# Kernel tuning notes

Measured on AMD Instinct MI355X. Metric: run time of the kernel, lower is better.

## Reference

```python
import jax, jax.numpy as jnp
import numpy as np

D_MODEL = 1024
NUM_HEADS = 16
DEPTH = D_MODEL // NUM_HEADS
NEG_INF = -1e9


def setup_inputs() -> dict:
    key = jax.random.key(0)
    ks = jax.random.split(key, 12)
    B, S = 4, 2048
    scale = 1.0 / np.sqrt(D_MODEL)
    inp = {
        "q": jax.random.normal(ks[0], (B, S, D_MODEL), jnp.float32),
        "k": jax.random.normal(ks[1], (B, S, D_MODEL), jnp.float32),
        "v": jax.random.normal(ks[2], (B, S, D_MODEL), jnp.float32),
        "mask": jax.random.randint(ks[3], (B, 1, 1, S), 0, 2, jnp.int32),
        "wq": jax.random.normal(ks[4], (D_MODEL, D_MODEL), jnp.float32) * scale,
        "bq": jnp.zeros((D_MODEL,), jnp.float32),
        "wk": jax.random.normal(ks[5], (D_MODEL, D_MODEL), jnp.float32) * scale,
        "bk": jnp.zeros((D_MODEL,), jnp.float32),
        "wv": jax.random.normal(ks[6], (D_MODEL, D_MODEL), jnp.float32) * scale,
        "bv": jnp.zeros((D_MODEL,), jnp.float32),
        "wo": jax.random.normal(ks[7], (D_MODEL, D_MODEL), jnp.float32) * scale,
        "bo": jnp.zeros((D_MODEL,), jnp.float32),
    }
    return inp


def _split_heads(x):
    # [B, S, D] -> [B, H, S, depth]
    B, S, _ = x.shape
    return x.reshape(B, S, NUM_HEADS, DEPTH).transpose(0, 2, 1, 3)


def reference(q, k, v, mask, wq, bq, wk, bk, wv, bv, wo, bo):
    B, S, _ = q.shape
    qh = _split_heads(q @ wq + bq)  # [B,H,S,d]
    kh = _split_heads(k @ wk + bk)
    vh = _split_heads(v @ wv + bv)
    logits = jnp.einsum("bhqd,bhkd->bhqk", qh, kh) / jnp.sqrt(
        jnp.asarray(DEPTH, jnp.float32))
    logits = logits + mask.astype(jnp.float32) * NEG_INF
    weights = jax.nn.softmax(logits, axis=-1)
    attn = jnp.einsum("bhqk,bhkd->bhqd", weights, vh)
    attn = attn.transpose(0, 2, 1, 3).reshape(B, S, D_MODEL)
    return attn @ wo + bo
```

## Files before the change

kernel.cpp:

```cpp
#include <hip/hip_runtime.h>

#define SB 4
#define SS 2048
#define SD 1024
#define SH 16

typedef float f32x4 __attribute__((ext_vector_type(4)));
typedef __bf16 bf16x8 __attribute__((ext_vector_type(8)));
typedef short short4v __attribute__((ext_vector_type(4)));
typedef unsigned int uint2v __attribute__((ext_vector_type(2)));

__device__ __forceinline__ unsigned short f2bf_(float x) {
    unsigned u = __builtin_bit_cast(unsigned, x);
    unsigned r = u + 0x7FFFu + ((u >> 16) & 1u);
    return (unsigned short)(r >> 16);
}

#define GL2LDS(g, l) __builtin_amdgcn_global_load_lds( \
    (const __attribute__((address_space(1))) unsigned int*)(g), \
    (__attribute__((address_space(3))) unsigned int*)(l), 16, 0, 0)

__global__ __launch_bounds__(256) void maskprep(
        const int* __restrict__ mk, float* __restrict__ MA, int n) {
    int i = blockIdx.x * 256 + threadIdx.x;
    if (i < n)
        MA[i] = (float)mk[i] * (-1e9f * 1.4426950408889634f) - 8.0f;
}

__global__ __launch_bounds__(256) void transpose4(
        const float* __restrict__ w0, const float* __restrict__ w1,
        const float* __restrict__ w2, const float* __restrict__ w3,
        unsigned short* __restrict__ out) {
    __shared__ unsigned short tile[32][33];
    int zz = blockIdx.z;
    const float* src = (zz == 0) ? w0 : (zz == 1) ? w1 : (zz == 2) ? w2 : w3;
    unsigned short* dst = out + (size_t)zz * 1024 * 1024;
    int x = blockIdx.x * 32 + threadIdx.x;
    int y0 = blockIdx.y * 32;
    for (int j = threadIdx.y; j < 32; j += 8)
        tile[j][threadIdx.x] = f2bf_(src[(size_t)(y0 + j) * 1024 + x]);
    __syncthreads();
    int ox = y0 + threadIdx.x;
    int oy0 = blockIdx.x * 32;
    for (int j = threadIdx.y; j < 32; j += 8)
        dst[(size_t)(oy0 + j) * 1024 + ox] = tile[threadIdx.x][j];
}

__global__ __launch_bounds__(256) void gemm_qkv(
        const float* __restrict__ Aq, const float* __restrict__ Ak,
        const float* __restrict__ Avv, const unsigned short* __restrict__ WT,
        const float* __restrict__ bq, const float* __restrict__ bk,
        const float* __restrict__ bv, unsigned short* __restrict__ Qh,
        unsigned short* __restrict__ Kh, unsigned short* __restrict__ VTr,
        float qscl) {
    __shared__ alignas(16) float Asmf[2][128][32];
    __shared__ alignas(16) unsigned short Bsm[2][128][32];
    const int zone = blockIdx.x >> 6;
    const int m0 = (blockIdx.x & 63) * 128, n0 = blockIdx.y * 128;
    const float* Af = (zone == 0) ? Aq : (zone == 1) ? Ak : Avv;
    const unsigned short* BT = WT + (size_t)zone * 1048576;
    const float* bias = (zone == 0) ? bq : (zone == 1) ? bk : bv;
    const int K = 1024, N = 1024;

    const int lane = threadIdx.x & 63, wid = threadIdx.x >> 6;
    const int wr = wid >> 1, wc = wid & 1;
    const int lr = lane >> 2;
    const int lco = (lane & 3) * 8;
    const int cl = lane & 15, kg = lane >> 4;

    f32x4 acc[4][4] = {};

    auto STAGE = [&](int buf, int k0) {
#pragma unroll
        for (int i = 0; i < 4; ++i) {
            int base = i * 32 + wid * 8;
            int row = base + (lane >> 3);
            int cs = (lane & 7) ^ (row & 7);
            GL2LDS(Af + (size_t)(m0 + row) * K + k0 + cs * 4, &Asmf[buf][base][0]);
        }
#pragma unroll
        for (int i = 0; i < 2; ++i) {
            int base = (i * 4 + wid) * 16;
            GL2LDS(BT + (size_t)(n0 + base + lr) * K + k0 + lco, &Bsm[buf][base][0]);
        }
    };

    STAGE(0, 0);
    __syncthreads();

    for (int k0 = 0; k0 < K; k0 += 32) {
        int cur = (k0 >> 5) & 1;
        if (k0 + 32 < K) STAGE(cur ^ 1, k0 + 32);

        bf16x8 af[4], bfv[4];
#pragma unroll
        for (int mi = 0; mi < 4; ++mi) {
            int r = wr * 64 + mi * 16 + cl;
            const float* Ar = &Asmf[cur][r][0];
            f32x4 a0 = *(const f32x4*)(Ar + ((2 * kg) ^ (r & 7)) * 4);
            f32x4 a1 = *(const f32x4*)(Ar + ((2 * kg + 1) ^ (r & 7)) * 4);
#pragma unroll
            for (int e = 0; e < 4; ++e) {
                af[mi][e] = (__bf16)a0[e];
                af[mi][4 + e] = (__bf16)a1[e];
            }
        }
#pragma unroll
        for (int ni = 0; ni < 4; ++ni)
            bfv[ni] = *(const bf16x8*)&Bsm[cur][wc * 64 + ni * 16 + cl][kg * 8];
#pragma unroll
        for (int mi = 0; mi < 4; ++mi)
#pragma unroll
            for (int ni = 0; ni < 4; ++ni)
                acc[mi][ni] = __builtin_amdgcn_mfma_f32_16x16x32_bf16(
                    af[mi], bfv[ni], acc[mi][ni], 0, 0, 0);
        __syncthreads();
    }

    const int rl = (lane >> 4) * 4;
    float os = (zone == 0) ? qscl : 1.0f;
#pragma unroll
    for (int mi = 0; mi < 4; ++mi) {
#pragma unroll
        for (int ni = 0; ni < 4; ++ni) {
            int row = m0 + wr * 64 + mi * 16 + rl;
            int col = n0 + wc * 64 + ni * 16 + cl;
            float bvv = bias[col];
            f32x4 v = acc[mi][ni];
            if (zone < 2) {
                unsigned short* C = (zone == 0) ? Qh : Kh;
#pragma unroll
                for (int j = 0; j < 4; ++j)
                    C[(size_t)(row + j) * N + col] = f2bf_((v[j] + bvv) * os);
            } else {
                int bb = row >> 11, s = row & 2047;
                short4v pk;
#pragma unroll
                for (int j = 0; j < 4; ++j)
                    pk[j] = (short)f2bf_(v[j] + bvv);
                *(short4v*)&VTr[((size_t)(bb * 1024 + col)) * 2048 + s] = pk;
            }
        }
    }
}

__global__ __launch_bounds__(256) void gemm_out(
        const unsigned short* __restrict__ Ab, const unsigned short* __restrict__ BT,
        const float* __restrict__ bias, float* __restrict__ C,
        int M, int N, int K) {
    __shared__ alignas(16) unsigned short Asmb[2][128][32];
    __shared__ alignas(16) unsigned short Bsm[2][128][32];
    const int m0 = blockIdx.x * 128, n0 = blockIdx.y * 128;
    const int lane = threadIdx.x & 63, wid = threadIdx.x >> 6;
    const int wr = wid >> 1, wc = wid & 1;
    const int lr = lane >> 2;
    const int lco = (lane & 3) * 8;
    const int cl = lane & 15, kg = lane >> 4;

    f32x4 acc[4][4] = {};

    auto STAGE = [&](int buf, int k0) {
#pragma unroll
        for (int i = 0; i < 2; ++i) {
            int base = (i * 4 + wid) * 16;
            GL2LDS(Ab + (size_t)(m0 + base + lr) * K + k0 + lco, &Asmb[buf][base][0]);
            GL2LDS(BT + (size_t)(n0 + base + lr) * K + k0 + lco, &Bsm[buf][base][0]);
        }
    };

    STAGE(0, 0);
    __syncthreads();

    for (int k0 = 0; k0 < K; k0 += 32) {
        int cur = (k0 >> 5) & 1;
        if (k0 + 32 < K) STAGE(cur ^ 1, k0 + 32);

        bf16x8 af[4], bfv[4];
#pragma unroll
        for (int mi = 0; mi < 4; ++mi)
            af[mi] = *(const bf16x8*)&Asmb[cur][wr * 64 + mi * 16 + cl][kg * 8];
#pragma unroll
        for (int ni = 0; ni < 4; ++ni)
            bfv[ni] = *(const bf16x8*)&Bsm[cur][wc * 64 + ni * 16 + cl][kg * 8];
#pragma unroll
        for (int mi = 0; mi < 4; ++mi)
#pragma unroll
            for (int ni = 0; ni < 4; ++ni)
                acc[mi][ni] = __builtin_amdgcn_mfma_f32_16x16x32_bf16(
                    af[mi], bfv[ni], acc[mi][ni], 0, 0, 0);
        __syncthreads();
    }

    const int rl = (lane >> 4) * 4;
#pragma unroll
    for (int mi = 0; mi < 4; ++mi) {
#pragma unroll
        for (int ni = 0; ni < 4; ++ni) {
            int row = m0 + wr * 64 + mi * 16 + rl;
            int col = n0 + wc * 64 + ni * 16 + cl;
            float bv = bias[col];
            f32x4 v = acc[mi][ni];
#pragma unroll
            for (int j = 0; j < 4; ++j)
                C[(size_t)(row + j) * N + col] = v[j] + bv;
        }
    }
}

__global__ __launch_bounds__(512) void attn_kernel(
        const unsigned short* __restrict__ Qp, const unsigned short* __restrict__ Kp,
        const unsigned short* __restrict__ VT, const float* __restrict__ MA,
        unsigned short* __restrict__ O) {
    __shared__ alignas(16) unsigned short Klds[2][128][64];
    __shared__ alignas(16) unsigned short Vlds[2][64][128];
    const int lane = threadIdx.x & 63, wid = threadIdx.x >> 6;
    const int bh = blockIdx.x;
    const int b = bh >> 4, h = bh & 15;
    const int qt = blockIdx.y;
    const int qrow0 = qt * 256 + wid * 32;
    const int cl = lane & 15, kg = lane >> 4;

    bf16x8 qf[2][2];
#pragma unroll
    for (int qh = 0; qh < 2; ++qh)
#pragma unroll
        for (int kh = 0; kh < 2; ++kh)
            qf[qh][kh] = *(const bf16x8*)&Qp[(size_t)(b * SS + qrow0 + qh * 16 + cl) * SD
                                            + h * 64 + kh * 32 + kg * 8];

    const float* MAb = MA + b * SS;

    f32x4 oacc[2][4] = {};
    f32x4 lsum[2] = {};

    auto STAGE = [&](int buf, int tt) {
        int kt = (tt & 15) * 128;
        {
            int r8 = lane >> 3, c8 = lane & 7;
#pragma unroll
            for (int i = 0; i < 2; ++i) {
                int r = i * 64 + wid * 8 + r8;
                int cs = c8 ^ (r & 7);
                GL2LDS(Kp + (size_t)(b * SS + kt + r) * SD + h * 64 + cs * 8,
                       &Klds[buf][i * 64 + wid * 8][0]);
            }
        }
        {
            int r16 = lane >> 4, c16 = lane & 15;
#pragma unroll
            for (int i = 0; i < 2; ++i) {
                int r = i * 32 + wid * 4 + r16;
                int cs = (c16 & 8) | ((c16 & 7) ^ (r & 7));
                GL2LDS(VT + (size_t)(b * 1024 + h * 64 + r) * 2048 + kt + cs * 8,
                       &Vlds[buf][i * 32 + wid * 4][0]);
            }
        }
    };

    auto QKCOL = [&](int buf, int kt, int cf, f32x4* sv) {
        int r = cf * 16 + cl;
        bf16x8 kf0 = *(const bf16x8*)&Klds[buf][r][((0 + kg) ^ (r & 7)) * 8];
        bf16x8 kf1 = *(const bf16x8*)&Klds[buf][r][((4 + kg) ^ (r & 7)) * 8];
        f32x4 M = *(const f32x4*)&MAb[kt + cf * 16 + 4 * kg];
        __builtin_amdgcn_s_setprio(1);
#pragma unroll
        for (int qh = 0; qh < 2; ++qh) {
            f32x4 s = {};
            s = __builtin_amdgcn_mfma_f32_16x16x32_bf16(kf0, qf[qh][0], s, 0, 0, 0);
            s = __builtin_amdgcn_mfma_f32_16x16x32_bf16(kf1, qf[qh][1], s, 0, 0, 0);
#pragma unroll
            for (int j = 0; j < 4; ++j)
                s[j] = __builtin_amdgcn_exp2f(s[j] + M[j]);
            sv[qh] = s;
            lsum[qh] += s;
        }
        __builtin_amdgcn_s_setprio(0);
    };

    auto STEP = [&](int buf, int t) {
        int kt = t * 128;
#pragma unroll
        for (int ks = 0; ks < 4; ++ks) {
            f32x4 sA[2], sB[2];
            QKCOL(buf, kt, ks, sA);
            QKCOL(buf, kt, ks + 4, sB);
            bf16x8 pa[2];
#pragma unroll
            for (int qh = 0; qh < 2; ++qh) {
                pa[qh][0] = (__bf16)sA[qh][0];
                pa[qh][1] = (__bf16)sA[qh][1];
                pa[qh][2] = (__bf16)sA[qh][2];
                pa[qh][3] = (__bf16)sA[qh][3];
                pa[qh][4] = (__bf16)sB[qh][0];
                pa[qh][5] = (__bf16)sB[qh][1];
                pa[qh][6] = (__bf16)sB[qh][2];
                pa[qh][7] = (__bf16)sB[qh][3];
            }
            __builtin_amdgcn_s_setprio(1);
#pragma unroll
            for (int nf = 0; nf < 4; ++nf) {
                int d = nf * 16 + cl;
                int c16a = 2 * ks + (kg >> 1);
                int c16b = 2 * (ks + 4) + (kg >> 1);
                int cha = (c16a & 8) | ((c16a & 7) ^ (d & 7));
                int chb = (c16b & 8) | ((c16b & 7) ^ (d & 7));
                const char* vb = (const char*)&Vlds[buf][d][0];
                uint2v lo = *(const uint2v*)(vb + cha * 16 + (kg & 1) * 8);
                uint2v hi = *(const uint2v*)(vb + chb * 16 + (kg & 1) * 8);
                bf16x8 vf;
                *(uint2v*)&vf = lo;
                *((uint2v*)&vf + 1) = hi;
#pragma unroll
                for (int qh = 0; qh < 2; ++qh)
                    oacc[qh][nf] = __builtin_amdgcn_mfma_f32_16x16x32_bf16(
                        pa[qh], vf, oacc[qh][nf], 0, 0, 0);
            }
            __builtin_amdgcn_s_setprio(0);
        }
    };

    STAGE(0, 0);
    __syncthreads();
    for (int t = 0; t < 16; ++t) {
        int cur = t & 1;
        STAGE(cur ^ 1, t + 1);
        STEP(cur, t);
        __syncthreads();
    }

    float lfull[2];
#pragma unroll
    for (int qh = 0; qh < 2; ++qh) {
        float l = (lsum[qh][0] + lsum[qh][1]) + (lsum[qh][2] + lsum[qh][3]);
        l += __shfl_xor(l, 16);
        l += __shfl_xor(l, 32);
        lfull[qh] = l;
    }
#pragma unroll
    for (int qh = 0; qh < 2; ++qh) {
#pragma unroll
        for (int j = 0; j < 4; ++j) {
            float inv = 1.0f / __shfl(lfull[qh], 4 * kg + j);
#pragma unroll
            for (int nf = 0; nf < 4; ++nf)
                O[(size_t)(b * SS + qrow0 + qh * 16 + 4 * kg + j) * SD + h * 64 + nf * 16 + cl] =
                    f2bf_(oacc[qh][nf][j] * inv);
        }
    }
}

extern "C" void kernel_launch(void* const* d_in, const int* in_sizes, int n_in,
                              void* d_out, int out_size, void* d_ws, size_t ws_size,
                              hipStream_t stream) {
    const float* q  = (const float*)d_in[0];
    const float* k  = (const float*)d_in[1];
    const float* v  = (const float*)d_in[2];
    const int*   mk = (const int*)d_in[3];
    const float* wq = (const float*)d_in[4];
    const float* bq = (const float*)d_in[5];
    const float* wk = (const float*)d_in[6];
    const float* bk = (const float*)d_in[7];
    const float* wv = (const float*)d_in[8];
    const float* bv = (const float*)d_in[9];
    const float* wo = (const float*)d_in[10];
    const float* bo = (const float*)d_in[11];
    float* out = (float*)d_out;

    char* ws = (char*)d_ws;
    unsigned short* WT  = (unsigned short*)ws;
    unsigned short* X   = (unsigned short*)(ws + 8388608);
    unsigned short* Qh  = (unsigned short*)(ws + 25165824);
    unsigned short* Kh  = (unsigned short*)(ws + 41943040);
    unsigned short* VTr = (unsigned short*)(ws + 58720256);
    float*          MAf = (float*)(ws + 75497472);

    const float QSCL = 0.125f * 1.4426950408889634f;

    transpose4<<<dim3(32, 32, 4), dim3(32, 8), 0, stream>>>(wq, wk, wv, wo, WT);
    maskprep<<<dim3(32), dim3(256), 0, stream>>>(mk, MAf, SB * SS);

    gemm_qkv<<<dim3(192, 8), dim3(256), 0, stream>>>(
        q, k, v, WT, bq, bk, bv, Qh, Kh, VTr, QSCL);

    attn_kernel<<<dim3(64, 8), dim3(512), 0, stream>>>(Qh, Kh, VTr, MAf, X);

    gemm_out<<<dim3(64, 8), dim3(256), 0, stream>>>(
        X, WT + 3 * 1048576, bo, out, 8192, 1024, 1024);
}
```

Measured before the change: 214.5 us.

## Swizzle bf16 LDS tiles and split fused QKV GEMM into three templated launches

```diff
diff --git a/kernel.cpp b/kernel.cpp
--- a/kernel.cpp
+++ b/kernel.cpp
@@ -46,26 +46,17 @@
         dst[(size_t)(oy0 + j) * 1024 + ox] = tile[threadIdx.x][j];
 }
 
-__global__ __launch_bounds__(256) void gemm_qkv(
-        const float* __restrict__ Aq, const float* __restrict__ Ak,
-        const float* __restrict__ Avv, const unsigned short* __restrict__ WT,
-        const float* __restrict__ bq, const float* __restrict__ bk,
-        const float* __restrict__ bv, unsigned short* __restrict__ Qh,
-        unsigned short* __restrict__ Kh, unsigned short* __restrict__ VTr,
-        float qscl) {
+template <int STORE_MODE>
+__global__ __launch_bounds__(256) void gemm_proj(
+        const float* __restrict__ Af, const unsigned short* __restrict__ BT,
+        const float* __restrict__ bias, unsigned short* __restrict__ C,
+        float oscale) {
+    const int K = 1024, N = 1024;
     __shared__ alignas(16) float Asmf[2][128][32];
     __shared__ alignas(16) unsigned short Bsm[2][128][32];
-    const int zone = blockIdx.x >> 6;
-    const int m0 = (blockIdx.x & 63) * 128, n0 = blockIdx.y * 128;
-    const float* Af = (zone == 0) ? Aq : (zone == 1) ? Ak : Avv;
-    const unsigned short* BT = WT + (size_t)zone * 1048576;
-    const float* bias = (zone == 0) ? bq : (zone == 1) ? bk : bv;
-    const int K = 1024, N = 1024;
-
+    const int m0 = blockIdx.x * 128, n0 = blockIdx.y * 128;
     const int lane = threadIdx.x & 63, wid = threadIdx.x >> 6;
     const int wr = wid >> 1, wc = wid & 1;
-    const int lr = lane >> 2;
-    const int lco = (lane & 3) * 8;
     const int cl = lane & 15, kg = lane >> 4;
 
     f32x4 acc[4][4] = {};
@@ -81,7 +72,9 @@
 #pragma unroll
         for (int i = 0; i < 2; ++i) {
             int base = (i * 4 + wid) * 16;
-            GL2LDS(BT + (size_t)(n0 + base + lr) * K + k0 + lco, &Bsm[buf][base][0]);
+            int row = base + (lane >> 2);
+            int cs = (lane & 3) ^ ((row >> 1) & 3);
+            GL2LDS(BT + (size_t)(n0 + row) * K + k0 + cs * 8, &Bsm[buf][base][0]);
         }
     };
 
@@ -106,8 +99,10 @@
             }
         }
 #pragma unroll
-        for (int ni = 0; ni < 4; ++ni)
-            bfv[ni] = *(const bf16x8*)&Bsm[cur][wc * 64 + ni * 16 + cl][kg * 8];
+        for (int ni = 0; ni < 4; ++ni) {
+            int r = wc * 64 + ni * 16 + cl;
+            bfv[ni] = *(const bf16x8*)&Bsm[cur][r][(kg ^ ((r >> 1) & 3)) * 8];
+        }
 #pragma unroll
         for (int mi = 0; mi < 4; ++mi)
 #pragma unroll
@@ -118,27 +113,25 @@
     }
 
     const int rl = (lane >> 4) * 4;
-    float os = (zone == 0) ? qscl : 1.0f;
 #pragma unroll
     for (int mi = 0; mi < 4; ++mi) {
 #pragma unroll
         for (int ni = 0; ni < 4; ++ni) {
             int row = m0 + wr * 64 + mi * 16 + rl;
             int col = n0 + wc * 64 + ni * 16 + cl;
-            float bvv = bias[col];
+            float bv = bias[col];
             f32x4 v = acc[mi][ni];
-            if (zone < 2) {
-                unsigned short* C = (zone == 0) ? Qh : Kh;
+            if (STORE_MODE == 0) {
 #pragma unroll
                 for (int j = 0; j < 4; ++j)
-                    C[(size_t)(row + j) * N + col] = f2bf_((v[j] + bvv) * os);
+                    C[(size_t)(row + j) * N + col] = f2bf_((v[j] + bv) * oscale);
             } else {
                 int bb = row >> 11, s = row & 2047;
                 short4v pk;
 #pragma unroll
                 for (int j = 0; j < 4; ++j)
-                    pk[j] = (short)f2bf_(v[j] + bvv);
-                *(short4v*)&VTr[((size_t)(bb * 1024 + col)) * 2048 + s] = pk;
+                    pk[j] = (short)f2bf_(v[j] + bv);
+                *(short4v*)&C[((size_t)(bb * 1024 + col)) * 2048 + s] = pk;
             }
         }
     }
@@ -153,8 +146,6 @@
     const int m0 = blockIdx.x * 128, n0 = blockIdx.y * 128;
     const int lane = threadIdx.x & 63, wid = threadIdx.x >> 6;
     const int wr = wid >> 1, wc = wid & 1;
-    const int lr = lane >> 2;
-    const int lco = (lane & 3) * 8;
     const int cl = lane & 15, kg = lane >> 4;
 
     f32x4 acc[4][4] = {};
@@ -163,8 +154,10 @@
 #pragma unroll
         for (int i = 0; i < 2; ++i) {
             int base = (i * 4 + wid) * 16;
-            GL2LDS(Ab + (size_t)(m0 + base + lr) * K + k0 + lco, &Asmb[buf][base][0]);
-            GL2LDS(BT + (size_t)(n0 + base + lr) * K + k0 + lco, &Bsm[buf][base][0]);
+            int row = base + (lane >> 2);
+            int cs = (lane & 3) ^ ((row >> 1) & 3);
+            GL2LDS(Ab + (size_t)(m0 + row) * K + k0 + cs * 8, &Asmb[buf][base][0]);
+            GL2LDS(BT + (size_t)(n0 + row) * K + k0 + cs * 8, &Bsm[buf][base][0]);
         }
     };
 
@@ -177,11 +170,15 @@
 
         bf16x8 af[4], bfv[4];
 #pragma unroll
-        for (int mi = 0; mi < 4; ++mi)
-            af[mi] = *(const bf16x8*)&Asmb[cur][wr * 64 + mi * 16 + cl][kg * 8];
-#pragma unroll
-        for (int ni = 0; ni < 4; ++ni)
-            bfv[ni] = *(const bf16x8*)&Bsm[cur][wc * 64 + ni * 16 + cl][kg * 8];
+        for (int mi = 0; mi < 4; ++mi) {
+            int r = wr * 64 + mi * 16 + cl;
+            af[mi] = *(const bf16x8*)&Asmb[cur][r][(kg ^ ((r >> 1) & 3)) * 8];
+        }
+#pragma unroll
+        for (int ni = 0; ni < 4; ++ni) {
+            int r = wc * 64 + ni * 16 + cl;
+            bfv[ni] = *(const bf16x8*)&Bsm[cur][r][(kg ^ ((r >> 1) & 3)) * 8];
+        }
 #pragma unroll
         for (int mi = 0; mi < 4; ++mi)
 #pragma unroll
@@ -379,8 +376,11 @@
     transpose4<<<dim3(32, 32, 4), dim3(32, 8), 0, stream>>>(wq, wk, wv, wo, WT);
     maskprep<<<dim3(32), dim3(256), 0, stream>>>(mk, MAf, SB * SS);
 
-    gemm_qkv<<<dim3(192, 8), dim3(256), 0, stream>>>(
-        q, k, v, WT, bq, bk, bv, Qh, Kh, VTr, QSCL);
+    dim3 gg(64, 8), gb(256);
+
+    gemm_proj<0><<<gg, gb, 0, stream>>>(q, WT,               bq, Qh,  QSCL);
+    gemm_proj<0><<<gg, gb, 0, stream>>>(k, WT + 1048576,     bk, Kh,  1.0f);
+    gemm_proj<1><<<gg, gb, 0, stream>>>(v, WT + 2 * 1048576, bv, VTr, 1.0f);
 
     attn_kernel<<<dim3(64, 8), dim3(512), 0, stream>>>(Qh, Kh, VTr, MAf, X);
 
```

Result: no change. 214.0 us (-0.2%).
